# Performance work log

Measured on AMD Instinct MI355X. Metric: run time of the kernel, lower is better.

The kernel has to match this reference:

```python
import jax, jax.numpy as jnp
import numpy as np

EPS = 1e-6

def setup_inputs() -> dict:
    key = jax.random.key(0)
    ks = jax.random.split(key, 9)
    B, T, D = 4, 1024, 128
    sc = 1.0 / np.sqrt(D)
    return {
        "x_seq": jax.random.normal(ks[0], (B, T, D), dtype=jnp.float32),
        "Wq": jax.random.uniform(ks[1], (D, D), jnp.float32, -sc, sc),
        "bq": jax.random.uniform(ks[2], (D,), jnp.float32, -sc, sc),
        "Wk": jax.random.uniform(ks[3], (D, D), jnp.float32, -sc, sc),
        "bk": jax.random.uniform(ks[4], (D,), jnp.float32, -sc, sc),
        "Wv": jax.random.uniform(ks[5], (D, D), jnp.float32, -sc, sc),
        "bv": jax.random.uniform(ks[6], (D,), jnp.float32, -sc, sc),
        "Wa": jax.random.uniform(ks[7], (D, D), jnp.float32, -sc, sc),
        "ba": jax.random.uniform(ks[8], (D,), jnp.float32, -sc, sc),
    }

def reference(x_seq, Wq, bq, Wk, bk, Wv, bv, Wa, ba):
    B, T, D = x_seq.shape
    q = jax.nn.relu(x_seq @ Wq.T + bq)          # [B,T,D]
    k = jax.nn.relu(x_seq @ Wk.T + bk)
    v = x_seq @ Wv.T + bv
    A = jax.nn.sigmoid(x_seq @ Wa.T + ba)       # per-step decay gate

    def step(carry, inp):
        s, z = carry                             # s:[B,D,D], z:[B,D]
        a_t, k_t, v_t, q_t = inp                 # each [B,D]
        s = a_t[:, :, None] * s + k_t[:, :, None] * v_t[:, None, :]  # s[b,i,j]=a_i*s + k_i v_j
        z = a_t * z + k_t
        num = jnp.einsum('bi,bij->bj', q_t, s)
        den = jnp.sum(q_t * z, axis=-1, keepdims=True) + EPS
        return (s, z), num / den

    s0 = jnp.zeros((B, D, D), x_seq.dtype)
    z0 = jnp.zeros((B, D), x_seq.dtype)
    xs = (jnp.swapaxes(A, 0, 1), jnp.swapaxes(k, 0, 1),
          jnp.swapaxes(v, 0, 1), jnp.swapaxes(q, 0, 1))  # time-major [T,B,D]
    _, y = jax.lax.scan(step, (s0, z0), xs)
    return jnp.swapaxes(y, 0, 1)                 # [B,T,D]
```

## Files before the change

### kernel.cpp

```cpp
#include <hip/hip_runtime.h>

#define BB 4
#define TT 1024
#define DD 128
#define LL 16
#define CC 64
#define EPSV 1e-6f

#define BTD (BB*TT*DD)
#define BCD (BB*CC*DD)

#define OFF_QC   0
#define OFF_KH   (OFF_QC + BTD)
#define OFF_V    (OFF_KH + BTD)
#define OFF_G    (OFF_V  + BTD)
#define OFF_CL   (OFF_G  + BTD)
#define OFF_KS   (OFF_CL + BCD)
#define OFF_Z0   (OFF_KS + BCD)
#define OFF_U    (OFF_Z0 + BCD)
#define OFF_S0   (OFF_U  + BB*CC*DD*DD)

__global__ __launch_bounds__(256) void k_gemm(
    const float* __restrict__ x,
    const float* __restrict__ Wq, const float* __restrict__ bq,
    const float* __restrict__ Wk, const float* __restrict__ bk,
    const float* __restrict__ Wv, const float* __restrict__ bv,
    const float* __restrict__ Wa, const float* __restrict__ ba,
    float* __restrict__ ws)
{
    __shared__ float xs [32][DD];
    __shared__ float wsh[64][132];

    const int tid = threadIdx.x;
    const int bx  = blockIdx.x;
    const int rt  = bx >> 3;
    const int mt  = bx & 7;
    const int m   = mt >> 1;
    const int jh  = mt & 1;

    const float* W    = (m==0)?Wq : (m==1)?Wk : (m==2)?Wv : Wa;
    const float* bias = (m==0)?bq : (m==1)?bk : (m==2)?bv : ba;

    {
        const float4* xg = (const float4*)(x + (size_t)rt*32*DD);
        #pragma unroll
        for (int r=0;r<4;r++){
            int f = tid + r*256;
            *(float4*)&xs[f>>5][(f&31)*4] = xg[f];
        }
        const float4* wg = (const float4*)(W + (size_t)jh*64*DD);
        #pragma unroll
        for (int r=0;r<8;r++){
            int f = tid + r*256;
            *(float4*)&wsh[f>>5][(f&31)*4] = wg[f];
        }
    }
    __syncthreads();

    const int ci = tid & 15;
    const int ri = tid >> 4;

    float acc[2][4];
    #pragma unroll
    for (int cc=0;cc<4;cc++){
        float bv_ = bias[jh*64 + ci + 16*cc];
        acc[0][cc]=bv_; acc[1][cc]=bv_;
    }

    #pragma unroll 2
    for (int k4=0; k4<32; k4++){
        float4 xa = *(const float4*)&xs[ri   ][k4*4];
        float4 xb = *(const float4*)&xs[ri+16][k4*4];
        #pragma unroll
        for (int cc=0;cc<4;cc++){
            float4 w = *(const float4*)&wsh[ci+16*cc][k4*4];
            acc[0][cc] = fmaf(xa.x,w.x, fmaf(xa.y,w.y, fmaf(xa.z,w.z, fmaf(xa.w,w.w, acc[0][cc]))));
            acc[1][cc] = fmaf(xb.x,w.x, fmaf(xb.y,w.y, fmaf(xb.z,w.z, fmaf(xb.w,w.w, acc[1][cc]))));
        }
    }

    float* dst = ws + ((m==0)?OFF_QC : (m==1)?OFF_KH : (m==2)?OFF_V : OFF_G);
    #pragma unroll
    for (int rr=0;rr<2;rr++){
        int row = rt*32 + ri + 16*rr;
        #pragma unroll
        for (int cc=0;cc<4;cc++){
            float v = acc[rr][cc];
            if (m==0 || m==1) v = fmaxf(v, 0.f);
            else if (m==3)    v = 1.f/(1.f+__expf(-v));
            dst[(size_t)row*DD + jh*64 + ci + 16*cc] = v;
        }
    }
}

__global__ __launch_bounds__(256) void k_chunk(float* __restrict__ ws)
{
    __shared__ float qs [LL][64];
    __shared__ float krs[LL][64];
    __shared__ float gs [LL][64];
    __shared__ float vs [LL][DD];
    __shared__ float kbs[LL][64];

    const int tid = threadIdx.x;
    const int bh  = blockIdx.x;
    const int bc  = bh >> 1;
    const int h   = bh & 1;
    const int ibase = h*64;
    const int b   = bc / CC;
    const int t0  = (bc % CC) * LL;
    const size_t tile = (size_t)(b*TT + t0)*DD;

    {
        const int t = tid >> 4, c4 = (tid & 15)*4;
        const size_t off = tile + (size_t)t*DD + ibase + c4;
        *(float4*)&qs [t][c4] = *(const float4*)(ws + OFF_QC + off);
        *(float4*)&krs[t][c4] = *(const float4*)(ws + OFF_KH + off);
        *(float4*)&gs [t][c4] = *(const float4*)(ws + OFF_G  + off);
        const int tv = tid >> 5, cv = (tid & 31)*4;
        *(float4*)&vs[tv  ][cv] = *(const float4*)(ws + OFF_V + tile + (size_t)tv*DD + cv);
        *(float4*)&vs[tv+8][cv] = *(const float4*)(ws + OFF_V + tile + (size_t)(tv+8)*DD + cv);
    }
    __syncthreads();

    if (tid < 64){
        float c = 1.f;
        #pragma unroll
        for (int t=0;t<LL;t++){ c *= gs[t][tid]; gs[t][tid] = c; }
        ws[OFF_CL + (size_t)bc*DD + ibase + tid] = c;
    }
    __syncthreads();

    {
        const int col = tid & 63;
        const int tg  = tid >> 6;
        const float cl = gs[LL-1][col];
        #pragma unroll
        for (int r=0;r<4;r++){
            int t = tg*4 + r;
            float cv = gs[t][col];
            ws[OFF_QC + tile + (size_t)t*DD + ibase + col] = qs[t][col] * cv;
            float kh = krs[t][col] / cv;
            ws[OFF_KH + tile + (size_t)t*DD + ibase + col] = kh;
            kbs[t][col] = kh * cl;
        }
    }
    __syncthreads();

    if (tid < 64){
        float s = 0.f;
        #pragma unroll
        for (int t=0;t<LL;t++) s += kbs[t][tid];
        ws[OFF_KS + (size_t)bc*DD + ibase + tid] = s;
    }

    const int j  = tid & 127;
    const int ih = tid >> 7;
    float vr[LL];
    #pragma unroll
    for (int u=0;u<LL;u++) vr[u]=vs[u][j];
    float* Ug = ws + OFF_U + (size_t)bc*DD*DD;
    #pragma unroll
    for (int i4=0;i4<8;i4++){
        int il = ih*32 + i4*4;
        float a0=0.f,a1=0.f,a2=0.f,a3=0.f;
        #pragma unroll
        for (int u=0;u<LL;u++){
            float4 kb4 = *(const float4*)(&kbs[u][il]);
            float vu = vr[u];
            a0 = fmaf(kb4.x,vu,a0); a1 = fmaf(kb4.y,vu,a1);
            a2 = fmaf(kb4.z,vu,a2); a3 = fmaf(kb4.w,vu,a3);
        }
        Ug[(size_t)(ibase+il+0)*DD + j]=a0; Ug[(size_t)(ibase+il+1)*DD + j]=a1;
        Ug[(size_t)(ibase+il+2)*DD + j]=a2; Ug[(size_t)(ibase+il+3)*DD + j]=a3;
    }
}

__global__ __launch_bounds__(128) void k_scan(float* __restrict__ ws)
{
    __shared__ float cls[CC], kss[CC];
    const int bi = blockIdx.x;
    const int b  = bi >> 7;
    const int i  = bi & 127;
    const int j  = threadIdx.x;

    if (j < CC) cls[j]      = ws[OFF_CL + (size_t)(b*CC + j)*DD + i];
    else        kss[j - CC] = ws[OFF_KS + (size_t)(b*CC + j - CC)*DD + i];
    __syncthreads();

    const float* U  = ws + OFF_U;
    float*       s0 = ws + OFF_S0;
    float*       z0 = ws + OFF_Z0;
    const size_t base = (size_t)b*CC*DD*DD + (size_t)i*DD + j;

    float up[16];
    #pragma unroll
    for (int p=0;p<16;p++) up[p] = U[base + (size_t)p*DD*DD];

    float s = 0.f, z = 0.f;
    #pragma unroll
    for (int ch=0; ch<CC; ch++){
        s0[base + (size_t)ch*DD*DD] = s;
        if (j==0) z0[(size_t)(b*CC+ch)*DD + i] = z;
        float u  = up[ch & 15];
        if (ch + 16 < CC) up[ch & 15] = U[base + (size_t)(ch+16)*DD*DD];
        float cl = cls[ch];
        s = fmaf(cl, s, u);
        z = fmaf(cl, z, kss[ch]);
    }
}

__global__ __launch_bounds__(256) void k_out(const float* __restrict__ ws, float* __restrict__ y)
{
    __shared__ float qcs[LL][DD+4];
    __shared__ float khs[LL][DD+4];
    __shared__ float vsm[LL][64+4];
    __shared__ float Ss[LL][LL];
    __shared__ float denS[LL];
    __shared__ float z0s[DD];
    __shared__ float s0s[2][32][64+4];

    const int tid = threadIdx.x;
    const int bh  = blockIdx.x;
    const int bc  = bh >> 1;
    const int jh  = bh & 1;
    const int jbase = jh * 64;
    const int b   = bc / CC;
    const int ch  = bc % CC;
    const int t0  = ch * LL;
    const size_t tile = (size_t)(b*TT + t0)*DD;
    const float* s0g = ws + OFF_S0 + (size_t)bc*DD*DD;

    float4 pre[2];
    {
        const float4* qcg = (const float4*)(ws + OFF_QC + tile);
        const float4* khg = (const float4*)(ws + OFF_KH + tile);
        #pragma unroll
        for (int rep=0; rep<2; rep++){
            int f = tid + rep*256;
            int t = f >> 5, k4 = f & 31;
            *(float4*)&qcs[t][k4*4] = qcg[f];
            *(float4*)&khs[t][k4*4] = khg[f];
        }
        {
            int t = tid >> 4, c = (tid & 15)*4;
            *(float4*)&vsm[t][c] =
                *(const float4*)(ws + OFF_V + tile + (size_t)t*DD + jbase + c);
        }
        if (tid < DD) z0s[tid] = ws[OFF_Z0 + (size_t)bc*DD + tid];
        #pragma unroll
        for (int r=0;r<2;r++){
            int f = tid + r*256;
            int row = f >> 4, c4 = (f & 15)*4;
            pre[r] = *(const float4*)(s0g + (size_t)row*DD + jbase + c4);
        }
    }
    __syncthreads();

    {
        int t = tid >> 4, u = tid & 15;
        float s = 0.f;
        #pragma unroll 8
        for (int k4=0; k4<32; k4++){
            float4 q4 = *(const float4*)&qcs[t][k4*4];
            float4 h4 = *(const float4*)&khs[u][k4*4];
            s = fmaf(q4.x,h4.x, fmaf(q4.y,h4.y, fmaf(q4.z,h4.z, fmaf(q4.w,h4.w, s))));
        }
        Ss[t][u] = (u <= t) ? s : 0.f;
    }
    __syncthreads();

    if (tid < LL){
        int t = tid;
        float d = EPSV;
        for (int u=0; u<=t; u++) d += Ss[t][u];
        #pragma unroll 8
        for (int kk=0; kk<DD; kk++) d += qcs[t][kk]*z0s[kk];
        denS[t] = d;
    }

    const int t  = tid >> 4;
    const int jg = tid & 15;
    const int j0 = jg * 4;
    float y4[4] = {0.f,0.f,0.f,0.f};

    __syncthreads();
    #pragma unroll
    for (int u=0; u<LL; u++){
        float sv = Ss[t][u];
        float4 v4 = *(const float4*)&vsm[u][j0];
        y4[0]=fmaf(sv,v4.x,y4[0]); y4[1]=fmaf(sv,v4.y,y4[1]);
        y4[2]=fmaf(sv,v4.z,y4[2]); y4[3]=fmaf(sv,v4.w,y4[3]);
    }

    #pragma unroll
    for (int sl=0; sl<4; sl++){
        __syncthreads();
        #pragma unroll
        for (int r=0;r<2;r++){
            int f = tid + r*256;
            *(float4*)&s0s[sl&1][f>>4][(f&15)*4] = pre[r];
        }
        if (sl < 3){
            #pragma unroll
            for (int r=0;r<2;r++){
                int f = tid + r*256;
                int row = f >> 4, c4 = (f & 15)*4;
                pre[r] = *(const float4*)(s0g + (size_t)((sl+1)*32 + row)*DD + jbase + c4);
            }
        }
        __syncthreads();
        #pragma unroll 8
        for (int ii=0; ii<32; ii++){
            float qv = qcs[t][sl*32+ii];
            float4 s4 = *(const float4*)&s0s[sl&1][ii][j0];
            y4[0]=fmaf(qv,s4.x,y4[0]); y4[1]=fmaf(qv,s4.y,y4[1]);
            y4[2]=fmaf(qv,s4.z,y4[2]); y4[3]=fmaf(qv,s4.w,y4[3]);
        }
    }

    const float rd = 1.f/denS[t];
    float* yg = y + tile + (size_t)t*DD + jbase + j0;
    *(float4*)yg = make_float4(y4[0]*rd, y4[1]*rd, y4[2]*rd, y4[3]*rd);
}

extern "C" void kernel_launch(void* const* d_in, const int* in_sizes, int n_in,
                              void* d_out, int out_size, void* d_ws, size_t ws_size,
                              hipStream_t stream)
{
    const float* x  = (const float*)d_in[0];
    const float* Wq = (const float*)d_in[1]; const float* bq = (const float*)d_in[2];
    const float* Wk = (const float*)d_in[3]; const float* bk = (const float*)d_in[4];
    const float* Wv = (const float*)d_in[5]; const float* bv = (const float*)d_in[6];
    const float* Wa = (const float*)d_in[7]; const float* ba = (const float*)d_in[8];
    float* ws = (float*)d_ws;
    float* yo = (float*)d_out;

    hipLaunchKernelGGL(k_gemm,  dim3(1024),    dim3(256), 0, stream,
                       x, Wq,bq, Wk,bk, Wv,bv, Wa,ba, ws);
    hipLaunchKernelGGL(k_chunk, dim3(BB*CC*2), dim3(256), 0, stream, ws);
    hipLaunchKernelGGL(k_scan,  dim3(BB*DD),   dim3(128), 0, stream, ws);
    hipLaunchKernelGGL(k_out,   dim3(BB*CC*2), dim3(256), 0, stream, ws, yo);
}
```

Baseline: 115.2 us.

## Double chunk length to 32 and split chunk/output kernels into quarter column blocks

Chunk length goes from 16 to 32, which halves the number of chunks. That halves the per-chunk state tensors U and S0 that are written and read through workspace, and shortens the serial inter-chunk scan. To keep the block count the same, the chunk and output kernels now split the feature dimension into four 32-wide slices instead of two 64-wide ones. The intra-chunk quadratic work doubles per chunk, and the register prefetch double-buffering of S0 in the output kernel is removed in favour of a simpler single-buffered load.

```diff
diff --git a/kernel.cpp b/kernel.cpp
--- a/kernel.cpp
+++ b/kernel.cpp
@@ -3,8 +3,8 @@
 #define BB 4
 #define TT 1024
 #define DD 128
-#define LL 16
-#define CC 64
+#define LL 32
+#define CC 32
 #define EPSV 1e-6f
 
 #define BTD (BB*TT*DD)
@@ -95,34 +95,37 @@
 
 __global__ __launch_bounds__(256) void k_chunk(float* __restrict__ ws)
 {
-    __shared__ float qs [LL][64];
-    __shared__ float krs[LL][64];
-    __shared__ float gs [LL][64];
+    __shared__ float qs [LL][32];
+    __shared__ float krs[LL][32];
+    __shared__ float gs [LL][32];
     __shared__ float vs [LL][DD];
-    __shared__ float kbs[LL][64];
+    __shared__ float kbs[LL][32];
 
     const int tid = threadIdx.x;
-    const int bh  = blockIdx.x;
-    const int bc  = bh >> 1;
-    const int h   = bh & 1;
-    const int ibase = h*64;
+    const int bq_ = blockIdx.x;
+    const int bc  = bq_ >> 2;
+    const int iq  = bq_ & 3;
+    const int ibase = iq*32;
     const int b   = bc / CC;
     const int t0  = (bc % CC) * LL;
     const size_t tile = (size_t)(b*TT + t0)*DD;
 
     {
-        const int t = tid >> 4, c4 = (tid & 15)*4;
+        const int t = tid >> 3, c4 = (tid & 7)*4;
         const size_t off = tile + (size_t)t*DD + ibase + c4;
         *(float4*)&qs [t][c4] = *(const float4*)(ws + OFF_QC + off);
         *(float4*)&krs[t][c4] = *(const float4*)(ws + OFF_KH + off);
         *(float4*)&gs [t][c4] = *(const float4*)(ws + OFF_G  + off);
-        const int tv = tid >> 5, cv = (tid & 31)*4;
-        *(float4*)&vs[tv  ][cv] = *(const float4*)(ws + OFF_V + tile + (size_t)tv*DD + cv);
-        *(float4*)&vs[tv+8][cv] = *(const float4*)(ws + OFF_V + tile + (size_t)(tv+8)*DD + cv);
-    }
-    __syncthreads();
-
-    if (tid < 64){
+        #pragma unroll
+        for (int r=0;r<4;r++){
+            int f = tid + r*256;
+            int tv = f >> 5, cv = (f & 31)*4;
+            *(float4*)&vs[tv][cv] = *(const float4*)(ws + OFF_V + tile + (size_t)tv*DD + cv);
+        }
+    }
+    __syncthreads();
+
+    if (tid < 32){
         float c = 1.f;
         #pragma unroll
         for (int t=0;t<LL;t++){ c *= gs[t][tid]; gs[t][tid] = c; }
@@ -131,8 +134,8 @@
     __syncthreads();
 
     {
-        const int col = tid & 63;
-        const int tg  = tid >> 6;
+        const int col = tid & 31;
+        const int tg  = tid >> 5;
         const float cl = gs[LL-1][col];
         #pragma unroll
         for (int r=0;r<4;r++){
@@ -146,7 +149,7 @@
     }
     __syncthreads();
 
-    if (tid < 64){
+    if (tid < 32){
         float s = 0.f;
         #pragma unroll
         for (int t=0;t<LL;t++) s += kbs[t][tid];
@@ -160,8 +163,8 @@
     for (int u=0;u<LL;u++) vr[u]=vs[u][j];
     float* Ug = ws + OFF_U + (size_t)bc*DD*DD;
     #pragma unroll
-    for (int i4=0;i4<8;i4++){
-        int il = ih*32 + i4*4;
+    for (int i4=0;i4<4;i4++){
+        int il = ih*16 + i4*4;
         float a0=0.f,a1=0.f,a2=0.f,a3=0.f;
         #pragma unroll
         for (int u=0;u<LL;u++){
@@ -183,8 +186,8 @@
     const int i  = bi & 127;
     const int j  = threadIdx.x;
 
-    if (j < CC) cls[j]      = ws[OFF_CL + (size_t)(b*CC + j)*DD + i];
-    else        kss[j - CC] = ws[OFF_KS + (size_t)(b*CC + j - CC)*DD + i];
+    if (j < CC)        cls[j]      = ws[OFF_CL + (size_t)(b*CC + j)*DD + i];
+    else if (j < 2*CC) kss[j - CC] = ws[OFF_KS + (size_t)(b*CC + j - CC)*DD + i];
     __syncthreads();
 
     const float* U  = ws + OFF_U;
@@ -213,59 +216,56 @@
 {
     __shared__ float qcs[LL][DD+4];
     __shared__ float khs[LL][DD+4];
-    __shared__ float vsm[LL][64+4];
+    __shared__ float vsm[LL][36];
     __shared__ float Ss[LL][LL];
     __shared__ float denS[LL];
     __shared__ float z0s[DD];
-    __shared__ float s0s[2][32][64+4];
+    __shared__ float s0s[32][36];
 
     const int tid = threadIdx.x;
-    const int bh  = blockIdx.x;
-    const int bc  = bh >> 1;
-    const int jh  = bh & 1;
-    const int jbase = jh * 64;
+    const int bq_ = blockIdx.x;
+    const int bc  = bq_ >> 2;
+    const int jq  = bq_ & 3;
+    const int jbase = jq * 32;
     const int b   = bc / CC;
     const int ch  = bc % CC;
     const int t0  = ch * LL;
     const size_t tile = (size_t)(b*TT + t0)*DD;
     const float* s0g = ws + OFF_S0 + (size_t)bc*DD*DD;
 
-    float4 pre[2];
     {
         const float4* qcg = (const float4*)(ws + OFF_QC + tile);
         const float4* khg = (const float4*)(ws + OFF_KH + tile);
         #pragma unroll
-        for (int rep=0; rep<2; rep++){
+        for (int rep=0; rep<4; rep++){
             int f = tid + rep*256;
             int t = f >> 5, k4 = f & 31;
             *(float4*)&qcs[t][k4*4] = qcg[f];
             *(float4*)&khs[t][k4*4] = khg[f];
         }
         {
-            int t = tid >> 4, c = (tid & 15)*4;
+            int t = tid >> 3, c = (tid & 7)*4;
             *(float4*)&vsm[t][c] =
                 *(const float4*)(ws + OFF_V + tile + (size_t)t*DD + jbase + c);
         }
         if (tid < DD) z0s[tid] = ws[OFF_Z0 + (size_t)bc*DD + tid];
-        #pragma unroll
-        for (int r=0;r<2;r++){
-            int f = tid + r*256;
-            int row = f >> 4, c4 = (f & 15)*4;
-            pre[r] = *(const float4*)(s0g + (size_t)row*DD + jbase + c4);
-        }
-    }
-    __syncthreads();
-
-    {
-        int t = tid >> 4, u = tid & 15;
-        float s = 0.f;
-        #pragma unroll 8
-        for (int k4=0; k4<32; k4++){
-            float4 q4 = *(const float4*)&qcs[t][k4*4];
-            float4 h4 = *(const float4*)&khs[u][k4*4];
-            s = fmaf(q4.x,h4.x, fmaf(q4.y,h4.y, fmaf(q4.z,h4.z, fmaf(q4.w,h4.w, s))));
-        }
-        Ss[t][u] = (u <= t) ? s : 0.f;
+    }
+    __syncthreads();
+
+    {
+        int t = tid >> 3, ug = tid & 7;
+        #pragma unroll
+        for (int uu=0; uu<4; uu++){
+            int u = ug*4 + uu;
+            float s = 0.f;
+            #pragma unroll 8
+            for (int k4=0; k4<32; k4++){
+                float4 q4 = *(const float4*)&qcs[t][k4*4];
+                float4 h4 = *(const float4*)&khs[u][k4*4];
+                s = fmaf(q4.x,h4.x, fmaf(q4.y,h4.y, fmaf(q4.z,h4.z, fmaf(q4.w,h4.w, s))));
+            }
+            Ss[t][u] = (u <= t) ? s : 0.f;
+        }
     }
     __syncthreads();
 
@@ -278,13 +278,13 @@
         denS[t] = d;
     }
 
-    const int t  = tid >> 4;
-    const int jg = tid & 15;
+    const int t  = tid >> 3;
+    const int jg = tid & 7;
     const int j0 = jg * 4;
     float y4[4] = {0.f,0.f,0.f,0.f};
 
     __syncthreads();
-    #pragma unroll
+    #pragma unroll 8
     for (int u=0; u<LL; u++){
         float sv = Ss[t][u];
         float4 v4 = *(const float4*)&vsm[u][j0];
@@ -292,27 +292,18 @@
         y4[2]=fmaf(sv,v4.z,y4[2]); y4[3]=fmaf(sv,v4.w,y4[3]);
     }
 
-    #pragma unroll
     for (int sl=0; sl<4; sl++){
         __syncthreads();
-        #pragma unroll
-        for (int r=0;r<2;r++){
-            int f = tid + r*256;
-            *(float4*)&s0s[sl&1][f>>4][(f&15)*4] = pre[r];
-        }
-        if (sl < 3){
-            #pragma unroll
-            for (int r=0;r<2;r++){
-                int f = tid + r*256;
-                int row = f >> 4, c4 = (f & 15)*4;
-                pre[r] = *(const float4*)(s0g + (size_t)((sl+1)*32 + row)*DD + jbase + c4);
-            }
+        {
+            int row = tid >> 3, c4 = (tid & 7)*4;
+            *(float4*)&s0s[row][c4] =
+                *(const float4*)(s0g + (size_t)(sl*32 + row)*DD + jbase + c4);
         }
         __syncthreads();
         #pragma unroll 8
         for (int ii=0; ii<32; ii++){
             float qv = qcs[t][sl*32+ii];
-            float4 s4 = *(const float4*)&s0s[sl&1][ii][j0];
+            float4 s4 = *(const float4*)&s0s[ii][j0];
             y4[0]=fmaf(qv,s4.x,y4[0]); y4[1]=fmaf(qv,s4.y,y4[1]);
             y4[2]=fmaf(qv,s4.z,y4[2]); y4[3]=fmaf(qv,s4.w,y4[3]);
         }
@@ -337,7 +328,7 @@
 
     hipLaunchKernelGGL(k_gemm,  dim3(1024),    dim3(256), 0, stream,
                        x, Wq,bq, Wk,bk, Wv,bv, Wa,ba, ws);
-    hipLaunchKernelGGL(k_chunk, dim3(BB*CC*2), dim3(256), 0, stream, ws);
+    hipLaunchKernelGGL(k_chunk, dim3(BB*CC*4), dim3(256), 0, stream, ws);
     hipLaunchKernelGGL(k_scan,  dim3(BB*DD),   dim3(128), 0, stream, ws);
-    hipLaunchKernelGGL(k_out,   dim3(BB*CC*2), dim3(256), 0, stream, ws, yo);
-}
+    hipLaunchKernelGGL(k_out,   dim3(BB*CC*4), dim3(256), 0, stream, ws, yo);
+}
```

Measured after the change: 118.5 us. +2.9%, slower.
